# Optimization experiments

Measured on AMD Instinct MI355X. Metric: run time of the kernel, lower is better.

Reference implementation:

```python
import math
import jax, jax.numpy as jnp
import numpy as np

EPS = 1e-06
NB_FEATURES = 256
NUM_HEADS = 16


def fwht(x):
    """Fast Walsh-Hadamard transform along last dim (power-of-two size)."""
    shape = x.shape
    P = shape[-1]
    h = 1
    while h < P:
        x = x.reshape(shape[:-1] + (-1, 2 * h))
        a, b = x[..., :h], x[..., h:]
        x = jnp.concatenate([a + b, a - b], axis=-1).reshape(shape)
        h *= 2
    return x


def apply_rope(q, k):
    # q,k: (C,H,L,D); RoPE applied to tokens 1..L-1, token 0 (condition) skipped
    C, H, L, D = q.shape
    dtype = q.dtype
    freqs = 10000.0 ** (-jnp.arange(0, D, 2, dtype=dtype) / D)  # (D/2,)
    pos = jnp.arange(L - 1, dtype=dtype)[:, None]               # (L-1,1)
    ang = pos * freqs                                            # (L-1,D/2)
    cos, sin = jnp.cos(ang), jnp.sin(ang)

    def rot(t):
        ts = t[..., 1:, :]
        t1, t2 = ts[..., 0::2], ts[..., 1::2]
        re = t1 * cos - t2 * sin
        im = t1 * sin + t2 * cos
        rs = jnp.stack([re, im], axis=-1).reshape(ts.shape)  # re-interleave even/odd
        return jnp.concatenate([t[..., :1, :], rs], axis=-2)

    return rot(q), rot(k)


def sorf_phi(x, signs, scales, m):
    # x: (C,H,L,D); signs: (H,R,3,P); scales: (H,R,P)
    C, H, L, D = x.shape
    R, P = signs.shape[1], signs.shape[-1]
    x_p = x if D == P else jnp.pad(x, ((0, 0), (0, 0), (0, 0), (0, P - D)))
    inv = 1.0 / math.sqrt(P)
    s1 = signs[None, :, :, 0, None, :]  # (1,H,R,1,P)
    s2 = signs[None, :, :, 1, None, :]
    s3 = signs[None, :, :, 2, None, :]
    g = (scales * inv)[None, :, :, None, :]  # (1,H,R,1,P)
    t = fwht(x_p[:, :, None, :, :] * s1) * inv  # (C,H,R,L,P)
    t = fwht(t * s2) * inv
    t = fwht(t * s3) * inv
    block = t * g
    phi = block.transpose(0, 1, 3, 2, 4).reshape(C, H, L, R * P)[..., :m]
    x_norm_sq = jnp.sum(x * x, axis=-1, keepdims=True) / 2.0
    return jnp.exp(phi - x_norm_sq) / math.sqrt(m)


def setup_inputs() -> dict:
    key = jax.random.key(0)
    ks = jax.random.split(key, 5)
    C, L, E = 4, 4096, 1024
    H, D = NUM_HEADS, 1024 // NUM_HEADS  # D = 64
    P = 64  # next power of two >= D
    R = 4   # ceil(256 / 64)
    x = jax.random.normal(ks[0], (C, L, E), dtype=jnp.float32)
    w_qkv = jax.random.normal(ks[1], (3 * E, E), dtype=jnp.float32) / math.sqrt(E)
    w_out = jax.random.normal(ks[2], (E, E), dtype=jnp.float32) / math.sqrt(E)
    sorf_signs = (2.0 * jax.random.randint(ks[3], (H, R, 3, P), 0, 2) - 1.0).astype(jnp.float32)
    sorf_scales = jax.random.normal(ks[4], (H, R, P), dtype=jnp.float32)
    return {"x": x, "w_qkv": w_qkv, "w_out": w_out,
            "sorf_signs": sorf_signs, "sorf_scales": sorf_scales}


def reference(x, w_qkv, w_out, sorf_signs, sorf_scales):
    C, L, E = x.shape
    H = NUM_HEADS
    D = E // H
    qkv = x @ w_qkv.T  # (C,L,3E)
    q, k, v = jnp.split(qkv, 3, axis=-1)
    to_heads = lambda t: t.reshape(C, L, H, D).transpose(0, 2, 1, 3)  # (C,H,L,D)
    q, k, v = to_heads(q), to_heads(k), to_heads(v)
    q, k = apply_rope(q, k)
    q_phi = sorf_phi(q, sorf_signs, sorf_scales, NB_FEATURES)  # (C,H,L,m)
    k_phi = sorf_phi(k, sorf_signs, sorf_scales, NB_FEATURES)
    # non-causal linear attention aggregation
    S = jnp.einsum('chlm,chld->chmd', k_phi, v)       # (C,H,m,D)
    sum_k = jnp.sum(k_phi, axis=2)                    # (C,H,m)
    numer = jnp.einsum('chlm,chmd->chld', q_phi, S)   # (C,H,L,D)
    denom = jnp.maximum(jnp.einsum('chlm,chm->chl', q_phi, sum_k), EPS)
    out_heads = numer / denom[..., None]
    out = out_heads.transpose(0, 2, 1, 3).reshape(C, L, E)
    return out @ w_out.T
```

## Files before the change

kernel.cpp:

```cpp
#include <hip/hip_runtime.h>
#include <math.h>


#define LOG2_10000 13.287712379549449f
#define TCONST 15.201805f
#define SIGMA 0.0009765625f

typedef __attribute__((ext_vector_type(8))) _Float16 h8;
typedef __attribute__((ext_vector_type(4))) _Float16 h4;
typedef __attribute__((ext_vector_type(4))) float f32x4;

#define GLDS16(gptr, lptr) __builtin_amdgcn_global_load_lds( \
    (const __attribute__((address_space(1))) void*)(gptr),   \
    (__attribute__((address_space(3))) void*)(lptr), 16, 0, 0)

__global__ __launch_bounds__(256) void k_zero(float* __restrict__ p, size_t n) {
    size_t i = (size_t)blockIdx.x * 256 + threadIdx.x;
    const size_t st = (size_t)gridDim.x * 256;
    for (; i < n; i += st) p[i] = 0.0f;
}

__global__ __launch_bounds__(256) void k_cvt_xw(const float* __restrict__ x,
                                                const float* __restrict__ wqkv,
                                                const float* __restrict__ wout,
                                                _Float16* __restrict__ xh,
                                                _Float16* __restrict__ wh,
                                                _Float16* __restrict__ wob) {
    const size_t st = (size_t)gridDim.x * 256;
    const size_t nx = (size_t)16384 * 1024 / 4;
    for (size_t i = (size_t)blockIdx.x * 256 + threadIdx.x; i < nx; i += st) {
        float4 v = ((const float4*)x)[i];
        h4 o = {(_Float16)v.x, (_Float16)v.y, (_Float16)v.z, (_Float16)v.w};
        ((h4*)xh)[i] = o;
    }
    const size_t nw = (size_t)3072 * 1024 / 4;
    for (size_t i = (size_t)blockIdx.x * 256 + threadIdx.x; i < nw; i += st) {
        float4 v = ((const float4*)wqkv)[i];
        h4 o = {(_Float16)v.x, (_Float16)v.y, (_Float16)v.z, (_Float16)v.w};
        ((h4*)wh)[i] = o;
    }
    const size_t no = (size_t)1024 * 1024 / 4;
    for (size_t i = (size_t)blockIdx.x * 256 + threadIdx.x; i < no; i += st) {
        float4 v = ((const float4*)wout)[i];
        h4 o = {(_Float16)v.x, (_Float16)v.y, (_Float16)v.z, (_Float16)v.w};
        ((h4*)wob)[i] = o;
    }
}

__global__ __launch_bounds__(64) void k_build_atf(const float* __restrict__ signs,
                                                  const float* __restrict__ scales,
                                                  _Float16* __restrict__ atfG) {
    const int b = blockIdx.x;
    const int hh = b >> 2, r = b & 3;
    const int j = threadIdx.x;
    const float* s1 = signs + ((size_t)(hh * 4 + r) * 3 + 0) * 64;
    const float* s2 = s1 + 64;
    const float* s3 = s1 + 128;
    const float* sc = scales + (size_t)(hh * 4 + r) * 64;

    float v[64];
    const float s1j = s1[j];
#pragma unroll
    for (int p = 0; p < 64; ++p) v[p] = (p == j) ? s1j : 0.0f;
#pragma unroll
    for (int st = 1; st < 64; st <<= 1)
#pragma unroll
        for (int p = 0; p < 64; ++p)
            if (!(p & st)) { float a = v[p], bq = v[p | st]; v[p] = a + bq; v[p | st] = a - bq; }
#pragma unroll
    for (int p = 0; p < 64; ++p) v[p] *= s2[p];
#pragma unroll
    for (int st = 1; st < 64; st <<= 1)
#pragma unroll
        for (int p = 0; p < 64; ++p)
            if (!(p & st)) { float a = v[p], bq = v[p | st]; v[p] = a + bq; v[p | st] = a - bq; }
#pragma unroll
    for (int p = 0; p < 64; ++p) v[p] *= s3[p];
#pragma unroll
    for (int st = 1; st < 64; st <<= 1)
#pragma unroll
        for (int p = 0; p < 64; ++p)
            if (!(p & st)) { float a = v[p], bq = v[p | st]; v[p] = a + bq; v[p | st] = a - bq; }
#pragma unroll
    for (int p = 0; p < 64; ++p)
        atfG[((size_t)hh * 256 + r * 64 + p) * 64 + j] = (_Float16)(v[p] * sc[p] * (1.0f / 4096.0f));
}

__global__ __launch_bounds__(256) void k_qkv_f16(const _Float16* __restrict__ xh,
                                                 const _Float16* __restrict__ wh,
                                                 _Float16* __restrict__ qb,
                                                 _Float16* __restrict__ kb,
                                                 _Float16* __restrict__ vb,
                                                 float* __restrict__ nq,
                                                 float* __restrict__ nk,
                                                 int n_base) {
    __shared__ char smem[34816];
    _Float16* Ah = (_Float16*)smem;
    _Float16* Bh = Ah + 8192;
    _Float16* Ol = (_Float16*)smem;

    const int tid = threadIdx.x;
    const int lane = tid & 63, w = tid >> 6;
    const int lane16 = lane & 15, lrow = lane >> 4;
    const int wm = w >> 1, wn = w & 1;
    const int m0 = blockIdx.y * 128, n0 = n_base + blockIdx.x * 128;

    f32x4 acc[4][4];
    const f32x4 zz = {0.f, 0.f, 0.f, 0.f};
#pragma unroll
    for (int i = 0; i < 4; ++i)
#pragma unroll
        for (int j = 0; j < 4; ++j) acc[i][j] = zz;

    for (int kt = 0; kt < 1024; kt += 64) {
        __syncthreads();
#pragma unroll
        for (int j = 0; j < 4; ++j) {
            const int g = (w * 4 + j) * 64 + lane;
            const int row = g & 127, ks = g >> 7;
            GLDS16(xh + (size_t)(m0 + row) * 1024 + kt + ks * 8, Ah + g * 8);
            GLDS16(wh + (size_t)(n0 + row) * 1024 + kt + ks * 8, Bh + g * 8);
        }
        __syncthreads();
#pragma unroll
        for (int s = 0; s < 2; ++s) {
            const int kd = s * 4 + lrow;
            h8 af[4], bf[4];
#pragma unroll
            for (int i = 0; i < 4; ++i)
                af[i] = *(h8*)(Ah + (kd * 128 + wm * 64 + i * 16 + lane16) * 8);
#pragma unroll
            for (int j = 0; j < 4; ++j)
                bf[j] = *(h8*)(Bh + (kd * 128 + wn * 64 + j * 16 + lane16) * 8);
#pragma unroll
            for (int i = 0; i < 4; ++i)
#pragma unroll
                for (int j = 0; j < 4; ++j)
                    acc[i][j] = __builtin_amdgcn_mfma_f32_16x16x32_f16(af[i], bf[j], acc[i][j], 0, 0, 0);
        }
    }

    __syncthreads();
    const int sec = n0 >> 10;
    float freqj[4];
#pragma unroll
    for (int j = 0; j < 4; ++j) {
        const int colw = wn * 64 + j * 16 + lane16;
        freqj[j] = exp2f(-(float)((colw & 63) & ~1) * (LOG2_10000 / 64.0f));
    }

#pragma unroll
    for (int i = 0; i < 4; ++i) {
        float nsum[4] = {0.f, 0.f, 0.f, 0.f};
#pragma unroll
        for (int j = 0; j < 4; ++j) {
            const int colw = wn * 64 + j * 16 + lane16;
#pragma unroll
            for (int r = 0; r < 4; ++r) {
                float v = acc[i][j][r];
                const float partner = __shfl_xor(v, 1);
                const int gm = m0 + wm * 64 + i * 16 + lrow * 4 + r;
                const int l = gm & 4095;
                if (sec < 2 && l > 0) {
                    float sn, cs;
                    sincosf((float)(l - 1) * freqj[j], &sn, &cs);
                    v = v * cs + sn * ((lane & 1) ? partner : -partner);
                }
                const _Float16 hv = (_Float16)v;
                if (sec < 2) {
                    const float vr = (float)hv;
                    nsum[r] += vr * vr;
                }
                Ol[(wm * 64 + i * 16 + lrow * 4 + r) * 136 + colw] = hv;
            }
        }
        if (sec < 2) {
#pragma unroll
            for (int m = 1; m < 16; m <<= 1)
#pragma unroll
                for (int r = 0; r < 4; ++r) nsum[r] += __shfl_xor(nsum[r], m);
            if (lane16 == 0) {
                float* ntgt = (sec == 0) ? nq : nk;
                const int hh = ((unsigned)(n0 + wn * 64) >> 6) & 15;
#pragma unroll
                for (int r = 0; r < 4; ++r) {
                    const int gm = m0 + wm * 64 + i * 16 + lrow * 4 + r;
                    const int c = gm >> 12, l = gm & 4095;
                    ntgt[((size_t)(c * 16 + hh)) * 4096 + l] = 0.5f * nsum[r];
                }
            }
        }
    }
    __syncthreads();
    {
        const int row = tid >> 1, half = tid & 1;
        const int gm = m0 + row;
        const int c = gm >> 12, l = gm & 4095;
        const int hh = ((unsigned)(n0 + half * 64) >> 6) & 15;
        _Float16* tgt = (sec == 0) ? qb : (sec == 1) ? kb : vb;
        const size_t base = ((size_t)(c * 16 + hh) * 4096 + l) * 64;
#pragma unroll
        for (int q8 = 0; q8 < 8; ++q8)
            *(h8*)(tgt + base + q8 * 8) = *(h8*)(Ol + row * 136 + half * 64 + q8 * 8);
    }
}

__global__ __launch_bounds__(256) void k_minred(const float* __restrict__ nk,
                                                float* __restrict__ MG) {
    const int ch = blockIdx.x;
    const int tid = threadIdx.x;
    __shared__ float red[4];
    float v = 1e30f;
    for (int i = tid; i < 4096; i += 256) v = fminf(v, nk[(size_t)ch * 4096 + i]);
#pragma unroll
    for (int off = 32; off >= 1; off >>= 1) v = fminf(v, __shfl_down(v, off));
    if ((tid & 63) == 0) red[tid >> 6] = v;
    __syncthreads();
    if (tid == 0) MG[ch] = fminf(fminf(red[0], red[1]), fminf(red[2], red[3]));
}

__global__ __launch_bounds__(256) void k_kvstats(const _Float16* __restrict__ kb,
                                                 const _Float16* __restrict__ vb,
                                                 const float* __restrict__ nkG,
                                                 const _Float16* __restrict__ atfG,
                                                 const float* __restrict__ MG,
                                                 float* __restrict__ St,
                                                 float* __restrict__ sumk) {
    __shared__ char smem[29824];
    _Float16* kl = (_Float16*)smem;
    _Float16* vt = kl + 2048;
    _Float16* pt = vt + 2560;
    float* nks = (float*)(pt + 10240);

    const int tid = threadIdx.x;
    const int lane = tid & 63, w = tid >> 6;
    const int lane16 = lane & 15, lrow = lane >> 4;
    const int ch = blockIdx.x, split = blockIdx.y;
    const int h = ch & 15;
    const _Float16* atfH = atfG + (size_t)h * 16384;
    const float Mch = MG[ch];

    f32x4 Sacc[4][4];
    const f32x4 zz = {0.f, 0.f, 0.f, 0.f};
#pragma unroll
    for (int i = 0; i < 4; ++i)
#pragma unroll
        for (int j = 0; j < 4; ++j) Sacc[i][j] = zz;
    float skr[4][4] = {};

    for (int chunk = 0; chunk < 16; ++chunk) {
        const int l0 = split * 512 + chunk * 32;
        __syncthreads();
        {
            const int g = w * 64 + lane;
            GLDS16(kb + ((size_t)ch * 4096 + l0 + (g & 31)) * 64 + (g >> 5) * 8, kl + g * 8);
        }
        {
            const int l = tid >> 3, d0 = (tid & 7) * 8;
            const h8 vv = *(const h8*)(vb + ((size_t)ch * 4096 + l0 + l) * 64 + d0);
#pragma unroll
            for (int j = 0; j < 8; ++j) vt[(d0 + j) * 40 + l] = vv[j];
        }
        if (tid < 32) nks[tid] = nkG[(size_t)ch * 4096 + l0 + tid];
        __syncthreads();
        f32x4 p[4][2];
#pragma unroll
        for (int i = 0; i < 4; ++i) { p[i][0] = zz; p[i][1] = zz; }
#pragma unroll
        for (int ks = 0; ks < 2; ++ks) {
            const int kd = ks * 4 + lrow;
            h8 bfr[2];
#pragma unroll
            for (int nf = 0; nf < 2; ++nf)
                bfr[nf] = *(h8*)(kl + (kd * 32 + nf * 16 + lane16) * 8);
#pragma unroll
            for (int mf = 0; mf < 4; ++mf) {
                const int f = w * 64 + mf * 16 + lane16;
                const h8 a = *(const h8*)(atfH + (size_t)f * 64 + kd * 8);
#pragma unroll
                for (int nf = 0; nf < 2; ++nf)
                    p[mf][nf] = __builtin_amdgcn_mfma_f32_16x16x32_f16(a, bfr[nf], p[mf][nf], 0, 0, 0);
            }
        }
#pragma unroll
        for (int mf = 0; mf < 4; ++mf)
#pragma unroll
            for (int nf = 0; nf < 2; ++nf) {
                const int ll = nf * 16 + lane16;
                const float nv = nks[ll];
#pragma unroll
                for (int r = 0; r < 4; ++r) {
                    const float e = expf(p[mf][nf][r] - nv + Mch);
                    skr[mf][r] += e;
                    const int fr = w * 64 + mf * 16 + lrow * 4 + r;
                    pt[fr * 40 + ll] = (_Float16)e;
                }
            }
        __syncthreads();
        h8 bfr2[4];
#pragma unroll
        for (int nf = 0; nf < 4; ++nf)
            bfr2[nf] = *(h8*)(pt + (w * 64 + nf * 16 + lane16) * 40 + lrow * 8);
#pragma unroll
        for (int mf = 0; mf < 4; ++mf) {
            const h8 a = *(h8*)(vt + (mf * 16 + lane16) * 40 + lrow * 8);
#pragma unroll
            for (int nf = 0; nf < 4; ++nf)
                Sacc[mf][nf] = __builtin_amdgcn_mfma_f32_16x16x32_f16(a, bfr2[nf], Sacc[mf][nf], 0, 0, 0);
        }
    }
#pragma unroll
    for (int mf = 0; mf < 4; ++mf)
#pragma unroll
        for (int nf = 0; nf < 4; ++nf)
#pragma unroll
            for (int r = 0; r < 4; ++r) {
                const int d = mf * 16 + lrow * 4 + r;
                const int f = w * 64 + nf * 16 + lane16;
                atomicAdd(&St[((size_t)ch * 64 + d) * 256 + f], Sacc[mf][nf][r]);
            }
#pragma unroll
    for (int mf = 0; mf < 4; ++mf) {
#pragma unroll
        for (int m = 1; m < 16; m <<= 1)
#pragma unroll
            for (int r = 0; r < 4; ++r) skr[mf][r] += __shfl_xor(skr[mf][r], m);
        if (lane16 == 0)
#pragma unroll
            for (int r = 0; r < 4; ++r)
                atomicAdd(&sumk[(size_t)ch * 256 + w * 64 + mf * 16 + lrow * 4 + r], skr[mf][r]);
    }
}

__global__ __launch_bounds__(256) void k_cvt_st(const float* __restrict__ St,
                                                const float* __restrict__ sumk,
                                                _Float16* __restrict__ Stb) {
    const size_t n = (size_t)64 * 80 * 256;
    const size_t st = (size_t)gridDim.x * 256;
    for (size_t e = (size_t)blockIdx.x * 256 + threadIdx.x; e < n; e += st) {
        const int f = (int)(e & 255);
        const int row = (int)((e >> 8) % 80);
        const int ch = (int)(e / (80 * 256));
        float v = 0.0f;
        if (row < 64) v = St[((size_t)ch * 64 + row) * 256 + f];
        else if (row == 64) v = sumk[(size_t)ch * 256 + f];
        Stb[e] = (_Float16)(v * SIGMA);
    }
}

__global__ __launch_bounds__(256) void k_attn(const _Float16* __restrict__ qb,
                                              const float* __restrict__ nqG,
                                              const _Float16* __restrict__ atfG,
                                              const _Float16* __restrict__ Stb,
                                              const float* __restrict__ MG,
                                              _Float16* __restrict__ oh) {
    __shared__ char smem[41216];
    _Float16* pq = (_Float16*)smem;
    _Float16* ql = pq + 16384;
    float* nqs = (float*)(ql + 4096);
    _Float16* olds = pq;

    const int tid = threadIdx.x;
    const int lane = tid & 63, w = tid >> 6;
    const int lane16 = lane & 15, lrow = lane >> 4;
    const int ch = blockIdx.x, lb = blockIdx.y;
    const int h = ch & 15, c = ch >> 4;
    const int l0 = lb * 64;
    const _Float16* atfH = atfG + (size_t)h * 16384;
    const _Float16* stbH = Stb + (size_t)ch * 20480;
    const float Mch = MG[ch];

#pragma unroll
    for (int j = 0; j < 2; ++j) {
        const int g = (w * 2 + j) * 64 + lane;
        GLDS16(qb + ((size_t)ch * 4096 + l0 + (g & 63)) * 64 + (g >> 6) * 8, ql + g * 8);
    }
    if (tid < 64) nqs[tid] = nqG[(size_t)ch * 4096 + l0 + tid];
    __syncthreads();

    const f32x4 zz = {0.f, 0.f, 0.f, 0.f};
    {
        f32x4 p[16];
#pragma unroll
        for (int nf = 0; nf < 16; ++nf) p[nf] = zz;
#pragma unroll
        for (int ks = 0; ks < 2; ++ks) {
            const int kd = ks * 4 + lrow;
            const h8 a = *(h8*)(ql + (kd * 64 + w * 16 + lane16) * 8);
#pragma unroll
            for (int nf = 0; nf < 16; ++nf) {
                const int f = nf * 16 + lane16;
                const h8 b = *(const h8*)(atfH + (size_t)f * 64 + kd * 8);
                p[nf] = __builtin_amdgcn_mfma_f32_16x16x32_f16(a, b, p[nf], 0, 0, 0);
            }
        }
#pragma unroll
        for (int nf = 0; nf < 16; ++nf) {
            const int f = nf * 16 + lane16;
#pragma unroll
            for (int r = 0; r < 4; ++r) {
                const float e = expf(p[nf][r]);
                const int l = w * 16 + lrow * 4 + r;
                pq[((f >> 3) * 64 + l) * 8 + (f & 7)] = (_Float16)e;
            }
        }
    }
    __syncthreads();
    f32x4 nacc[5];
#pragma unroll
    for (int nf = 0; nf < 5; ++nf) nacc[nf] = zz;
#pragma unroll
    for (int ks = 0; ks < 8; ++ks) {
        const int kd = ks * 4 + lrow;
        const h8 a = *(h8*)(pq + (kd * 64 + w * 16 + lane16) * 8);
#pragma unroll
        for (int nf = 0; nf < 5; ++nf) {
            const int dd = nf * 16 + lane16;
            const h8 b = *(const h8*)(stbH + (size_t)dd * 256 + kd * 8);
            nacc[nf] = __builtin_amdgcn_mfma_f32_16x16x32_f16(a, b, nacc[nf], 0, 0, 0);
        }
    }
    __syncthreads();
    {
#pragma unroll
        for (int r = 0; r < 4; ++r) {
            const float dn = __shfl(nacc[4][r], (lane & 48));
            const int row = w * 16 + lrow * 4 + r;
            const float t = expf(nqs[row] + Mch - TCONST);
            const float rden = 1.0f / fmaxf(dn, t);
#pragma unroll
            for (int nf = 0; nf < 4; ++nf)
                olds[row * 72 + nf * 16 + lane16] = (_Float16)(nacc[nf][r] * rden);
        }
    }
    __syncthreads();
    {
        const int row = tid >> 2, d0 = (tid & 3) * 16;
        const size_t base = ((size_t)c * 4096 + l0 + row) * 1024 + h * 64 + d0;
        *(h8*)(oh + base) = *(h8*)(olds + row * 72 + d0);
        *(h8*)(oh + base + 8) = *(h8*)(olds + row * 72 + d0 + 8);
    }
}

__global__ __launch_bounds__(256) void k_outgemm(const _Float16* __restrict__ OH,
                                                 const _Float16* __restrict__ WOB,
                                                 float* __restrict__ OUT) {
    __shared__ char smem[32768];
    _Float16* Asm = (_Float16*)smem;
    _Float16* Bsm = Asm + 8192;

    const int tid = threadIdx.x;
    const int lane = tid & 63, w = tid >> 6;
    const int lane16 = lane & 15, lrow = lane >> 4;
    const int wm = w >> 1, wn = w & 1;
    const int m0 = blockIdx.y * 128, n0 = blockIdx.x * 128;

    f32x4 acc[4][4];
    const f32x4 zz = {0.f, 0.f, 0.f, 0.f};
#pragma unroll
    for (int i = 0; i < 4; ++i)
#pragma unroll
        for (int j = 0; j < 4; ++j) acc[i][j] = zz;

    for (int kt = 0; kt < 1024; kt += 64) {
        __syncthreads();
#pragma unroll
        for (int j = 0; j < 4; ++j) {
            const int g = (w * 4 + j) * 64 + lane;
            const int row = g & 127, ks = g >> 7;
            GLDS16(OH + (size_t)(m0 + row) * 1024 + kt + ks * 8, Asm + g * 8);
            GLDS16(WOB + (size_t)(n0 + row) * 1024 + kt + ks * 8, Bsm + g * 8);
        }
        __syncthreads();
#pragma unroll
        for (int s = 0; s < 2; ++s) {
            const int kd = s * 4 + lrow;
            h8 af[4], bf[4];
#pragma unroll
            for (int i = 0; i < 4; ++i)
                af[i] = *(h8*)(Asm + (kd * 128 + wm * 64 + i * 16 + lane16) * 8);
#pragma unroll
            for (int j = 0; j < 4; ++j)
                bf[j] = *(h8*)(Bsm + (kd * 128 + wn * 64 + j * 16 + lane16) * 8);
#pragma unroll
            for (int i = 0; i < 4; ++i)
#pragma unroll
                for (int j = 0; j < 4; ++j)
                    acc[i][j] = __builtin_amdgcn_mfma_f32_16x16x32_f16(af[i], bf[j], acc[i][j], 0, 0, 0);
        }
    }
#pragma unroll
    for (int i = 0; i < 4; ++i)
#pragma unroll
        for (int j = 0; j < 4; ++j)
#pragma unroll
            for (int r = 0; r < 4; ++r) {
                const int gm = m0 + wm * 64 + i * 16 + lrow * 4 + r;
                const int gn = n0 + wn * 64 + j * 16 + lane16;
                OUT[(size_t)gm * 1024 + gn] = acc[i][j][r];
            }
}

extern "C" void kernel_launch(void* const* d_in, const int* in_sizes, int n_in,
                              void* d_out, int out_size, void* d_ws, size_t ws_size,
                              hipStream_t stream) {
    const float* x      = (const float*)d_in[0];
    const float* w_qkv  = (const float*)d_in[1];
    const float* w_out  = (const float*)d_in[2];
    const float* signs  = (const float*)d_in[3];
    const float* scales = (const float*)d_in[4];
    float* out = (float*)d_out;

    _Float16* hs = (_Float16*)d_ws;
    _Float16* xh  = hs;
    _Float16* wh  = xh + 16777216;
    _Float16* wob = wh + 3145728;
    _Float16* kb  = wob + 1048576;
    _Float16* vb  = kb + 16777216;
    _Float16* atf = vb + 16777216;
    _Float16* stb = atf + 262144;
    float* St   = (float*)(stb + 1310720);
    float* sumk = St + 1048576;
    float* nq   = sumk + 16384;
    float* nk   = nq + 262144;
    float* MG   = nk + 262144;
    _Float16* qb = kb;
    _Float16* oh = vb;

    k_cvt_xw<<<dim3(1024), dim3(256), 0, stream>>>(x, w_qkv, w_out, xh, wh, wob);
    k_build_atf<<<dim3(64), dim3(64), 0, stream>>>(signs, scales, atf);
    k_zero<<<dim3(1024), dim3(256), 0, stream>>>(St, (size_t)1048576 + 16384);
    k_qkv_f16<<<dim3(16, 128), dim3(256), 0, stream>>>(xh, wh, qb, kb, vb, nq, nk, 1024);
    k_minred<<<dim3(64), dim3(256), 0, stream>>>(nk, MG);
    k_kvstats<<<dim3(64, 8), dim3(256), 0, stream>>>(kb, vb, nk, atf, MG, St, sumk);
    k_cvt_st<<<dim3(1280), dim3(256), 0, stream>>>(St, sumk, stb);
    k_qkv_f16<<<dim3(8, 128), dim3(256), 0, stream>>>(xh, wh, qb, kb, vb, nq, nk, 0);
    k_attn<<<dim3(64, 64), dim3(256), 0, stream>>>(qb, nq, atf, stb, MG, oh);
    k_outgemm<<<dim3(8, 128), dim3(256), 0, stream>>>(oh, wob, out);
}
```

Measured before the change: 721.6 us.

## Double-buffer LDS tiles and remap blocks for XCD locality in GEMMs

Both the QKV and output GEMM kernels now prefetch the next K-tile into a second LDS buffer while MFMAs consume the current one, which removes one barrier per iteration and overlaps global-to-LDS loads with compute. The launch grid is flattened to 1D and block indices are swizzled across the 8 XCDs so that blocks sharing rows land on the same die's L2. LDS use per block roughly doubles to 64KB, which may cut occupancy. The epilogue's Ol overlay relies on the final barrier inside the loop.

```diff
diff --git a/kernel.cpp b/kernel.cpp
--- a/kernel.cpp
+++ b/kernel.cpp
@@ -93,17 +93,19 @@
                                                  _Float16* __restrict__ vb,
                                                  float* __restrict__ nq,
                                                  float* __restrict__ nk,
-                                                 int n_base) {
-    __shared__ char smem[34816];
-    _Float16* Ah = (_Float16*)smem;
-    _Float16* Bh = Ah + 8192;
+                                                 int n_base, int nbn) {
+    __shared__ char smem[65536];
     _Float16* Ol = (_Float16*)smem;
 
     const int tid = threadIdx.x;
     const int lane = tid & 63, w = tid >> 6;
     const int lane16 = lane & 15, lrow = lane >> 4;
     const int wm = w >> 1, wn = w & 1;
-    const int m0 = blockIdx.y * 128, n0 = n_base + blockIdx.x * 128;
+
+    const int per = gridDim.x >> 3;
+    const int sw = ((int)blockIdx.x & 7) * per + ((int)blockIdx.x >> 3);
+    const int bn = sw % nbn, bm = sw / nbn;
+    const int m0 = bm * 128, n0 = n_base + bn * 128;
 
     f32x4 acc[4][4];
     const f32x4 zz = {0.f, 0.f, 0.f, 0.f};
@@ -112,35 +114,55 @@
 #pragma unroll
         for (int j = 0; j < 4; ++j) acc[i][j] = zz;
 
-    for (int kt = 0; kt < 1024; kt += 64) {
-        __syncthreads();
-#pragma unroll
-        for (int j = 0; j < 4; ++j) {
-            const int g = (w * 4 + j) * 64 + lane;
+    {
+        _Float16* Ad = (_Float16*)smem;
+        _Float16* Bd = (_Float16*)smem + 16384;
+#pragma unroll
+        for (int s = 0; s < 4; ++s) {
+            const int g = s * 256 + tid;
             const int row = g & 127, ks = g >> 7;
-            GLDS16(xh + (size_t)(m0 + row) * 1024 + kt + ks * 8, Ah + g * 8);
-            GLDS16(wh + (size_t)(n0 + row) * 1024 + kt + ks * 8, Bh + g * 8);
-        }
-        __syncthreads();
+            GLDS16(xh + (size_t)(m0 + row) * 1024 + ks * 8, Ad + g * 8);
+            GLDS16(wh + (size_t)(n0 + row) * 1024 + ks * 8, Bd + g * 8);
+        }
+    }
+    __syncthreads();
+
+    int cur = 0;
+    for (int it = 0; it < 16; ++it) {
+        if (it < 15) {
+            const int kt = (it + 1) * 64;
+            _Float16* Ad = (_Float16*)smem + (cur ^ 1) * 8192;
+            _Float16* Bd = (_Float16*)smem + 16384 + (cur ^ 1) * 8192;
+#pragma unroll
+            for (int s = 0; s < 4; ++s) {
+                const int g = s * 256 + tid;
+                const int row = g & 127, ks = g >> 7;
+                GLDS16(xh + (size_t)(m0 + row) * 1024 + kt + ks * 8, Ad + g * 8);
+                GLDS16(wh + (size_t)(n0 + row) * 1024 + kt + ks * 8, Bd + g * 8);
+            }
+        }
+        const _Float16* Ah = (_Float16*)smem + cur * 8192;
+        const _Float16* Bh = (_Float16*)smem + 16384 + cur * 8192;
 #pragma unroll
         for (int s = 0; s < 2; ++s) {
             const int kd = s * 4 + lrow;
             h8 af[4], bf[4];
 #pragma unroll
             for (int i = 0; i < 4; ++i)
-                af[i] = *(h8*)(Ah + (kd * 128 + wm * 64 + i * 16 + lane16) * 8);
+                af[i] = *(const h8*)(Ah + (kd * 128 + wm * 64 + i * 16 + lane16) * 8);
 #pragma unroll
             for (int j = 0; j < 4; ++j)
-                bf[j] = *(h8*)(Bh + (kd * 128 + wn * 64 + j * 16 + lane16) * 8);
+                bf[j] = *(const h8*)(Bh + (kd * 128 + wn * 64 + j * 16 + lane16) * 8);
 #pragma unroll
             for (int i = 0; i < 4; ++i)
 #pragma unroll
                 for (int j = 0; j < 4; ++j)
                     acc[i][j] = __builtin_amdgcn_mfma_f32_16x16x32_f16(af[i], bf[j], acc[i][j], 0, 0, 0);
         }
-    }
-
-    __syncthreads();
+        __syncthreads();
+        cur ^= 1;
+    }
+
     const int sec = n0 >> 10;
     float freqj[4];
 #pragma unroll
@@ -445,15 +467,17 @@
 __global__ __launch_bounds__(256) void k_outgemm(const _Float16* __restrict__ OH,
                                                  const _Float16* __restrict__ WOB,
                                                  float* __restrict__ OUT) {
-    __shared__ char smem[32768];
-    _Float16* Asm = (_Float16*)smem;
-    _Float16* Bsm = Asm + 8192;
+    __shared__ char smem[65536];
 
     const int tid = threadIdx.x;
     const int lane = tid & 63, w = tid >> 6;
     const int lane16 = lane & 15, lrow = lane >> 4;
     const int wm = w >> 1, wn = w & 1;
-    const int m0 = blockIdx.y * 128, n0 = blockIdx.x * 128;
+
+    const int per = gridDim.x >> 3;
+    const int sw = ((int)blockIdx.x & 7) * per + ((int)blockIdx.x >> 3);
+    const int bn = sw & 7, bm = sw >> 3;
+    const int m0 = bm * 128, n0 = bn * 128;
 
     f32x4 acc[4][4];
     const f32x4 zz = {0.f, 0.f, 0.f, 0.f};
@@ -462,32 +486,53 @@
 #pragma unroll
         for (int j = 0; j < 4; ++j) acc[i][j] = zz;
 
-    for (int kt = 0; kt < 1024; kt += 64) {
-        __syncthreads();
-#pragma unroll
-        for (int j = 0; j < 4; ++j) {
-            const int g = (w * 4 + j) * 64 + lane;
+    {
+        _Float16* Ad = (_Float16*)smem;
+        _Float16* Bd = (_Float16*)smem + 16384;
+#pragma unroll
+        for (int s = 0; s < 4; ++s) {
+            const int g = s * 256 + tid;
             const int row = g & 127, ks = g >> 7;
-            GLDS16(OH + (size_t)(m0 + row) * 1024 + kt + ks * 8, Asm + g * 8);
-            GLDS16(WOB + (size_t)(n0 + row) * 1024 + kt + ks * 8, Bsm + g * 8);
-        }
-        __syncthreads();
+            GLDS16(OH + (size_t)(m0 + row) * 1024 + ks * 8, Ad + g * 8);
+            GLDS16(WOB + (size_t)(n0 + row) * 1024 + ks * 8, Bd + g * 8);
+        }
+    }
+    __syncthreads();
+
+    int cur = 0;
+    for (int it = 0; it < 16; ++it) {
+        if (it < 15) {
+            const int kt = (it + 1) * 64;
+            _Float16* Ad = (_Float16*)smem + (cur ^ 1) * 8192;
+            _Float16* Bd = (_Float16*)smem + 16384 + (cur ^ 1) * 8192;
+#pragma unroll
+            for (int s = 0; s < 4; ++s) {
+                const int g = s * 256 + tid;
+                const int row = g & 127, ks = g >> 7;
+                GLDS16(OH + (size_t)(m0 + row) * 1024 + kt + ks * 8, Ad + g * 8);
+                GLDS16(WOB + (size_t)(n0 + row) * 1024 + kt + ks * 8, Bd + g * 8);
+            }
+        }
+        const _Float16* Ah = (_Float16*)smem + cur * 8192;
+        const _Float16* Bh = (_Float16*)smem + 16384 + cur * 8192;
 #pragma unroll
         for (int s = 0; s < 2; ++s) {
             const int kd = s * 4 + lrow;
             h8 af[4], bf[4];
 #pragma unroll
             for (int i = 0; i < 4; ++i)
-                af[i] = *(h8*)(Asm + (kd * 128 + wm * 64 + i * 16 + lane16) * 8);
+                af[i] = *(const h8*)(Ah + (kd * 128 + wm * 64 + i * 16 + lane16) * 8);
 #pragma unroll
             for (int j = 0; j < 4; ++j)
-                bf[j] = *(h8*)(Bsm + (kd * 128 + wn * 64 + j * 16 + lane16) * 8);
+                bf[j] = *(const h8*)(Bh + (kd * 128 + wn * 64 + j * 16 + lane16) * 8);
 #pragma unroll
             for (int i = 0; i < 4; ++i)
 #pragma unroll
                 for (int j = 0; j < 4; ++j)
                     acc[i][j] = __builtin_amdgcn_mfma_f32_16x16x32_f16(af[i], bf[j], acc[i][j], 0, 0, 0);
         }
+        __syncthreads();
+        cur ^= 1;
     }
 #pragma unroll
     for (int i = 0; i < 4; ++i)
@@ -530,11 +575,11 @@
     k_cvt_xw<<<dim3(1024), dim3(256), 0, stream>>>(x, w_qkv, w_out, xh, wh, wob);
     k_build_atf<<<dim3(64), dim3(64), 0, stream>>>(signs, scales, atf);
     k_zero<<<dim3(1024), dim3(256), 0, stream>>>(St, (size_t)1048576 + 16384);
-    k_qkv_f16<<<dim3(16, 128), dim3(256), 0, stream>>>(xh, wh, qb, kb, vb, nq, nk, 1024);
+    k_qkv_f16<<<dim3(2048), dim3(256), 0, stream>>>(xh, wh, qb, kb, vb, nq, nk, 1024, 16);
     k_minred<<<dim3(64), dim3(256), 0, stream>>>(nk, MG);
     k_kvstats<<<dim3(64, 8), dim3(256), 0, stream>>>(kb, vb, nk, atf, MG, St, sumk);
     k_cvt_st<<<dim3(1280), dim3(256), 0, stream>>>(St, sumk, stb);
-    k_qkv_f16<<<dim3(8, 128), dim3(256), 0, stream>>>(xh, wh, qb, kb, vb, nq, nk, 0);
+    k_qkv_f16<<<dim3(1024), dim3(256), 0, stream>>>(xh, wh, qb, kb, vb, nq, nk, 0, 8);
     k_attn<<<dim3(64, 64), dim3(256), 0, stream>>>(qb, nq, atf, stb, MG, oh);
-    k_outgemm<<<dim3(8, 128), dim3(256), 0, stream>>>(oh, wob, out);
-}
+    k_outgemm<<<dim3(1024), dim3(256), 0, stream>>>(oh, wob, out);
+}
```

Result: no change. 709.3 us (-1.7%).
